# Performance work log

Hardware: AMD Instinct MI355X
Metric: run time of the kernel (lower is better)

## Reference

```python
import jax, jax.numpy as jnp
import numpy as np

N_NODES = 30000
N_EDGES = 480000
N_GRAPHS = 128
D_IN = 128
D_H = 256
N_CLASSES = 60


def gcn_conv(x, src, dst, norm, W, b, num_nodes):
    # x: [N, d_in]; W: [d_out, d_in]; b: [d_out]
    h = x @ W.T                                   # [N, d_out]
    msg = h[src] * norm[:, None]                  # [E+N, d_out] gather + scale
    out = jax.ops.segment_sum(msg, dst, num_segments=num_nodes)  # scatter-add
    return out + b


def setup_inputs() -> dict:
    key = jax.random.key(0)
    ks = jax.random.split(key, 10)
    glorot = lambda k, o, i: jax.random.normal(k, (o, i), jnp.float32) * (2.0 / (o + i)) ** 0.5
    x = jax.random.normal(ks[0], (N_NODES, D_IN), jnp.float32)
    edge_index = jax.random.randint(ks[1], (2, N_EDGES), 0, N_NODES, jnp.int64)
    batch = jnp.sort(jax.random.randint(ks[2], (N_NODES,), 0, N_GRAPHS, jnp.int64))
    return {
        "x": x,
        "edge_index": edge_index,
        "batch": batch,
        "W1": glorot(ks[3], D_H, D_IN), "b1": jnp.zeros((D_H,), jnp.float32),
        "W2": glorot(ks[4], D_H, D_H),  "b2": jnp.zeros((D_H,), jnp.float32),
        "W3": glorot(ks[5], D_H, D_H),  "b3": jnp.zeros((D_H,), jnp.float32),
        "Wfc": glorot(ks[6], N_CLASSES, D_H),
        "bfc": jnp.zeros((N_CLASSES,), jnp.float32),
    }


def reference(x, edge_index, batch, W1, b1, W2, b2, W3, b3, Wfc, bfc):
    num_nodes = x.shape[0]
    # GCNConv default: add self-loops, symmetric normalization D^-1/2 A D^-1/2
    loops = jnp.arange(num_nodes, dtype=edge_index.dtype)
    src = jnp.concatenate([edge_index[0], loops])
    dst = jnp.concatenate([edge_index[1], loops])
    deg = jax.ops.segment_sum(jnp.ones_like(dst, dtype=x.dtype), dst,
                              num_segments=num_nodes)
    dinv = jnp.where(deg > 0, jax.lax.rsqrt(deg), 0.0)
    norm = dinv[src] * dinv[dst]                  # per-edge normalization

    h = jax.nn.relu(gcn_conv(x, src, dst, norm, W1, b1, num_nodes))
    h = jax.nn.relu(gcn_conv(h, src, dst, norm, W2, b2, num_nodes))
    h = jax.nn.relu(gcn_conv(h, src, dst, norm, W3, b3, num_nodes))

    # global_mean_pool over graph ids
    sums = jax.ops.segment_sum(h, batch, num_segments=N_GRAPHS)
    cnts = jax.ops.segment_sum(jnp.ones((num_nodes,), h.dtype), batch,
                               num_segments=N_GRAPHS)
    pooled = sums / jnp.maximum(cnts, 1.0)[:, None]   # [G, 256]
    return pooled @ Wfc.T + bfc                       # [G, num_classes]
```

## Files before the change

### kernel.cpp

```cpp
#include <hip/hip_runtime.h>
#include <cstdint>
#include <cstddef>

#define NN 30000
#define NE 480000
#define NG 128
#define DIN 128
#define DH 256
#define NC 60
#define CAP 64
#define P1MAX (NN * DIN / 4)

typedef _Float16 f16x8 __attribute__((ext_vector_type(8)));
typedef _Float16 half4_t __attribute__((ext_vector_type(4)));
typedef float f32x4 __attribute__((ext_vector_type(4)));

__device__ __forceinline__ void gload_lds16(const _Float16* g, _Float16* l) {
    __builtin_amdgcn_global_load_lds(
        (const __attribute__((address_space(1))) void*)g,
        (__attribute__((address_space(3))) void*)l, 16, 0, 0);
}

__global__ __launch_bounds__(256) void k_pre(const int* __restrict__ ei, int* __restrict__ cursor,
        int* __restrict__ csr_src,
        const float* __restrict__ x, _Float16* __restrict__ xh,
        const float* __restrict__ W1, const float* __restrict__ W2, const float* __restrict__ W3,
        _Float16* __restrict__ w1h, _Float16* __restrict__ w2h, _Float16* __restrict__ w3h,
        float* __restrict__ sums) {
    int i = blockIdx.x * 256 + threadIdx.x;
    if (i < NE) {
        int s = ei[i];
        int d = ei[NE + i];
        int slot = atomicAdd(&cursor[d], 1);
        if (slot < CAP) csr_src[d * CAP + slot] = s;
    }
    if (i < P1MAX) {
        float4 v = ((const float4*)x)[i];
        half4_t o;
        o[0] = (_Float16)v.x; o[1] = (_Float16)v.y;
        o[2] = (_Float16)v.z; o[3] = (_Float16)v.w;
        ((half4_t*)xh)[i] = o;
    }
    if (i < DH * DIN) w1h[i] = (_Float16)W1[i];
    if (i < DH * DH) {
        w2h[i] = (_Float16)W2[i];
        w3h[i] = (_Float16)W3[i];
    }
    if (i < NG * DH) sums[i] = 0.f;
}

template<int K>
__global__ __launch_bounds__(256) void k_agg(const _Float16* __restrict__ hin,
        _Float16* __restrict__ tout, const int* __restrict__ cnt,
        const int* __restrict__ csr_src) {
    constexpr int L = K / 8;
    constexpr int G = 64 / L;
    int node = blockIdx.x * 4 + (threadIdx.x >> 6);
    int lane = threadIdx.x & 63;
    int sub = lane / L;
    int off = lane % L;
    const _Float16* gbase = hin + off * 8;
    float acc[8];
    #pragma unroll
    for (int u = 0; u < 8; u++) acc[u] = 0.f;
    int deg = cnt[node];
    float dvd = rsqrtf((float)(deg + 1));
    int c = deg < CAP ? deg : CAP;
    int beg = node * CAP, end = beg + c;
    int e = beg;
    for (; e + 4 * G <= end; e += 4 * G) {
        int s[4]; float w[4]; f16x8 r[4];
        #pragma unroll
        for (int j = 0; j < 4; j++) s[j] = csr_src[e + j * G + sub];
        #pragma unroll
        for (int j = 0; j < 4; j++) w[j] = rsqrtf((float)(cnt[s[j]] + 1)) * dvd;
        #pragma unroll
        for (int j = 0; j < 4; j++) r[j] = *(const f16x8*)(gbase + (size_t)s[j] * K);
        #pragma unroll
        for (int j = 0; j < 4; j++)
            #pragma unroll
            for (int u = 0; u < 8; u++) acc[u] = fmaf(w[j], (float)r[j][u], acc[u]);
    }
    for (; e < end; e += G) {
        int idx = e + sub;
        int s0 = node; float w0 = 0.f;
        if (idx < end) { s0 = csr_src[idx]; w0 = rsqrtf((float)(cnt[s0] + 1)) * dvd; }
        f16x8 r0 = *(const f16x8*)(gbase + (size_t)s0 * K);
        #pragma unroll
        for (int u = 0; u < 8; u++) acc[u] = fmaf(w0, (float)r0[u], acc[u]);
    }
    {
        float sws = (sub == 0) ? dvd * dvd : 0.f;
        f16x8 rs = *(const f16x8*)(gbase + (size_t)node * K);
        #pragma unroll
        for (int u = 0; u < 8; u++) acc[u] = fmaf(sws, (float)rs[u], acc[u]);
    }
    #pragma unroll
    for (int u = 0; u < 8; u++) {
        float v = acc[u];
        #pragma unroll
        for (int m = L; m < 64; m <<= 1) v += __shfl_xor(v, m, 64);
        acc[u] = v;
    }
    if (sub == 0) {
        f16x8 o;
        #pragma unroll
        for (int u = 0; u < 8; u++) o[u] = (_Float16)acc[u];
        *(f16x8*)(tout + (size_t)node * K + off * 8) = o;
    }
}

template<int K, bool FUSE_POOL>
__global__ __launch_bounds__(256) void k_gemm(const _Float16* __restrict__ A,
        const _Float16* __restrict__ W, const float* __restrict__ bias,
        _Float16* __restrict__ Cb, const int* __restrict__ batch,
        float* __restrict__ sums) {
    __shared__ __align__(16) _Float16 lsA[64 * 32];
    __shared__ __align__(16) _Float16 lsB[64 * 32];
    int t = threadIdx.x;
    int bm = blockIdx.x * 64;
    int bn = blockIdx.y * 64;
    int lane = t & 63, wv = t >> 6;
    int wm = (wv & 1) * 32;
    int wn = (wv >> 1) * 32;
    int lm = lane & 15, q = lane >> 4;
    int r4 = t >> 2;
    int c4 = t & 3;
    int ra = bm + r4; if (ra >= NN) ra = NN - 1;
    int rb = bn + r4;

    f32x4 acc[2][2];
    #pragma unroll
    for (int i = 0; i < 2; i++)
        #pragma unroll
        for (int j = 0; j < 2; j++) acc[i][j] = (f32x4){0.f, 0.f, 0.f, 0.f};

    for (int k0 = 0; k0 < K; k0 += 32) {
        size_t ko = (size_t)k0 + c4 * 8;
        __syncthreads();
        gload_lds16(A + (size_t)ra * K + ko, lsA + t * 8);
        gload_lds16(W + (size_t)rb * K + ko, lsB + t * 8);
        __syncthreads();
        f16x8 bf[2];
        #pragma unroll
        for (int nt = 0; nt < 2; nt++)
            bf[nt] = *(const f16x8*)&lsB[(wn + nt * 16 + lm) * 32 + q * 8];
        #pragma unroll
        for (int mt = 0; mt < 2; mt++) {
            f16x8 af = *(const f16x8*)&lsA[(wm + mt * 16 + lm) * 32 + q * 8];
            #pragma unroll
            for (int nt = 0; nt < 2; nt++)
                acc[mt][nt] = __builtin_amdgcn_mfma_f32_16x16x32_f16(af, bf[nt], acc[mt][nt], 0, 0, 0);
        }
    }
    if constexpr (!FUSE_POOL) {
        #pragma unroll
        for (int mt = 0; mt < 2; mt++) {
            #pragma unroll
            for (int nt = 0; nt < 2; nt++) {
                int col = bn + wn + nt * 16 + lm;
                float bv = bias[col];
                #pragma unroll
                for (int r = 0; r < 4; r++) {
                    int row = bm + wm + mt * 16 + q * 4 + r;
                    if (row < NN) {
                        float v = fmaxf(acc[mt][nt][r] + bv, 0.f);
                        Cb[(size_t)row * 256 + col] = (_Float16)v;
                    }
                }
            }
        }
    } else {
        int gid[8];
        #pragma unroll
        for (int mt = 0; mt < 2; mt++)
            #pragma unroll
            for (int r = 0; r < 4; r++) {
                int row = bm + wm + mt * 16 + q * 4 + r;
                gid[mt * 4 + r] = (row < NN) ? batch[row] : -1;
            }
        #pragma unroll
        for (int nt = 0; nt < 2; nt++) {
            int col = bn + wn + nt * 16 + lm;
            float bv = bias[col];
            float runsum = 0.f;
            int curg = -1;
            #pragma unroll
            for (int mt = 0; mt < 2; mt++) {
                #pragma unroll
                for (int r = 0; r < 4; r++) {
                    int g = gid[mt * 4 + r];
                    if (g >= 0) {
                        float v = fmaxf(acc[mt][nt][r] + bv, 0.f);
                        if (g != curg) {
                            if (curg >= 0) atomicAdd(&sums[curg * DH + col], runsum);
                            curg = g;
                            runsum = 0.f;
                        }
                        runsum += v;
                    }
                }
            }
            if (curg >= 0) atomicAdd(&sums[curg * DH + col], runsum);
        }
    }
}

__global__ __launch_bounds__(64) void k_fc(const float* __restrict__ sums,
        const int* __restrict__ batch, const float* __restrict__ Wfc,
        const float* __restrict__ bfc, float* __restrict__ out) {
    __shared__ float p[DH];
    int g = blockIdx.x;
    int t = threadIdx.x;
    int lo = 0, hi = NN;
    while (lo < hi) { int mid = (lo + hi) >> 1; if (batch[mid] < g) lo = mid + 1; else hi = mid; }
    int start = lo;
    hi = NN;
    while (lo < hi) { int mid = (lo + hi) >> 1; if (batch[mid] < g + 1) lo = mid + 1; else hi = mid; }
    int cnt = lo - start;
    float inv = (cnt > 0) ? 1.f / (float)cnt : 0.f;
    for (int i = t; i < DH; i += 64) p[i] = sums[g * DH + i] * inv;
    __syncthreads();
    if (t < NC) {
        float a = bfc[t];
        for (int k = 0; k < DH; k++) a = fmaf(p[k], Wfc[t * DH + k], a);
        out[g * NC + t] = a;
    }
}

extern "C" void kernel_launch(void* const* d_in, const int* in_sizes, int n_in,
                              void* d_out, int out_size, void* d_ws, size_t ws_size,
                              hipStream_t stream) {
    const float* x     = (const float*)d_in[0];
    const int*   ei    = (const int*)d_in[1];
    const int*   batch = (const int*)d_in[2];
    const float* W1 = (const float*)d_in[3];
    const float* b1 = (const float*)d_in[4];
    const float* W2 = (const float*)d_in[5];
    const float* b2 = (const float*)d_in[6];
    const float* W3 = (const float*)d_in[7];
    const float* b3 = (const float*)d_in[8];
    const float* Wfc = (const float*)d_in[9];
    const float* bfc = (const float*)d_in[10];
    float* out = (float*)d_out;

    char* wp = (char*)d_ws;
    auto alloc = [&](size_t bytes) {
        char* q = wp;
        wp += (bytes + 511) & ~(size_t)511;
        return (void*)q;
    };
    int*   cursor  = (int*)alloc((size_t)NN * 4);
    int*   csr_src = (int*)alloc((size_t)NN * CAP * 4);
    float* sums    = (float*)alloc((size_t)NG * DH * 4);
    _Float16* xh   = (_Float16*)alloc((size_t)NN * DIN * 2);
    _Float16* tb   = (_Float16*)alloc((size_t)NN * DH * 2);
    _Float16* hA   = (_Float16*)alloc((size_t)NN * DH * 2);
    _Float16* hB   = (_Float16*)alloc((size_t)NN * DH * 2);
    _Float16* w1h = (_Float16*)alloc((size_t)DH * DIN * 2);
    _Float16* w2h = (_Float16*)alloc((size_t)DH * DH * 2);
    _Float16* w3h = (_Float16*)alloc((size_t)DH * DH * 2);

    hipMemsetAsync(cursor, 0, (size_t)NN * 4, stream);

    k_pre<<<(P1MAX + 255) / 256, 256, 0, stream>>>(ei, cursor, csr_src, x, xh,
                                                   W1, W2, W3, w1h, w2h, w3h, sums);

    dim3 gg((NN + 63) / 64, 4);
    k_agg<128><<<NN / 4, 256, 0, stream>>>(xh, tb, cursor, csr_src);
    k_gemm<128, false><<<gg, 256, 0, stream>>>(tb, w1h, b1, hA, nullptr, nullptr);
    k_agg<256><<<NN / 4, 256, 0, stream>>>(hA, tb, cursor, csr_src);
    k_gemm<256, false><<<gg, 256, 0, stream>>>(tb, w2h, b2, hB, nullptr, nullptr);
    k_agg<256><<<NN / 4, 256, 0, stream>>>(hB, tb, cursor, csr_src);
    k_gemm<256, true><<<gg, 256, 0, stream>>>(tb, w3h, b3, nullptr, batch, sums);

    k_fc<<<NG, 64, 0, stream>>>(sums, batch, Wfc, bfc, out);
}
```

Before: 266.1 us.

## Split feature dimension across blocks in aggregation kernel with 8 edges per wavefront

The aggregation kernel now splits each node's feature vector into 64-wide slices, each handled by its own block. Every wavefront covers 8 features per lane and processes 8 edges in parallel with a 2-deep unroll, which gives more blocks and more edge-level parallelism per node. It also switches to nontemporal loads for CSR indices and nontemporal stores for outputs. In exchange, CSR indices and degree lookups are re-read once per slice, and the single-slice wave shape gives up the wider feature coverage per lane that K=128 had before.

```diff
diff --git a/kernel.cpp b/kernel.cpp
--- a/kernel.cpp
+++ b/kernel.cpp
@@ -53,13 +53,15 @@
 __global__ __launch_bounds__(256) void k_agg(const _Float16* __restrict__ hin,
         _Float16* __restrict__ tout, const int* __restrict__ cnt,
         const int* __restrict__ csr_src) {
-    constexpr int L = K / 8;
-    constexpr int G = 64 / L;
-    int node = blockIdx.x * 4 + (threadIdx.x >> 6);
+    constexpr int SL = K / 64;
+    int bid = blockIdx.x;
+    int slice = bid % SL;
+    int nb = bid / SL;
+    int node = nb * 4 + (threadIdx.x >> 6);
     int lane = threadIdx.x & 63;
-    int sub = lane / L;
-    int off = lane % L;
-    const _Float16* gbase = hin + off * 8;
+    int sub = lane >> 3;
+    int off = lane & 7;
+    const _Float16* gbase = hin + slice * 64 + off * 8;
     float acc[8];
     #pragma unroll
     for (int u = 0; u < 8; u++) acc[u] = 0.f;
@@ -67,27 +69,25 @@
     float dvd = rsqrtf((float)(deg + 1));
     int c = deg < CAP ? deg : CAP;
     int beg = node * CAP, end = beg + c;
-    int e = beg;
-    for (; e + 4 * G <= end; e += 4 * G) {
-        int s[4]; float w[4]; f16x8 r[4];
-        #pragma unroll
-        for (int j = 0; j < 4; j++) s[j] = csr_src[e + j * G + sub];
-        #pragma unroll
-        for (int j = 0; j < 4; j++) w[j] = rsqrtf((float)(cnt[s[j]] + 1)) * dvd;
-        #pragma unroll
-        for (int j = 0; j < 4; j++) r[j] = *(const f16x8*)(gbase + (size_t)s[j] * K);
-        #pragma unroll
-        for (int j = 0; j < 4; j++)
+    for (int e = beg; e < end; e += 16) {
+        int s[2]; float w[2]; f16x8 r[2];
+        #pragma unroll
+        for (int j = 0; j < 2; j++) {
+            int idx = e + j * 8 + sub;
+            s[j] = (idx < end) ? __builtin_nontemporal_load(&csr_src[idx]) : node;
+        }
+        #pragma unroll
+        for (int j = 0; j < 2; j++)
+            r[j] = *(const f16x8*)(gbase + (size_t)s[j] * K);
+        #pragma unroll
+        for (int j = 0; j < 2; j++) {
+            int idx = e + j * 8 + sub;
+            w[j] = (idx < end) ? rsqrtf((float)(cnt[s[j]] + 1)) * dvd : 0.f;
+        }
+        #pragma unroll
+        for (int j = 0; j < 2; j++)
             #pragma unroll
             for (int u = 0; u < 8; u++) acc[u] = fmaf(w[j], (float)r[j][u], acc[u]);
-    }
-    for (; e < end; e += G) {
-        int idx = e + sub;
-        int s0 = node; float w0 = 0.f;
-        if (idx < end) { s0 = csr_src[idx]; w0 = rsqrtf((float)(cnt[s0] + 1)) * dvd; }
-        f16x8 r0 = *(const f16x8*)(gbase + (size_t)s0 * K);
-        #pragma unroll
-        for (int u = 0; u < 8; u++) acc[u] = fmaf(w0, (float)r0[u], acc[u]);
     }
     {
         float sws = (sub == 0) ? dvd * dvd : 0.f;
@@ -99,14 +99,14 @@
     for (int u = 0; u < 8; u++) {
         float v = acc[u];
         #pragma unroll
-        for (int m = L; m < 64; m <<= 1) v += __shfl_xor(v, m, 64);
+        for (int m = 8; m < 64; m <<= 1) v += __shfl_xor(v, m, 64);
         acc[u] = v;
     }
     if (sub == 0) {
         f16x8 o;
         #pragma unroll
         for (int u = 0; u < 8; u++) o[u] = (_Float16)acc[u];
-        *(f16x8*)(tout + (size_t)node * K + off * 8) = o;
+        __builtin_nontemporal_store(o, (f16x8*)(tout + (size_t)node * K + slice * 64 + off * 8));
     }
 }
 
@@ -267,11 +267,11 @@
                                                    W1, W2, W3, w1h, w2h, w3h, sums);
 
     dim3 gg((NN + 63) / 64, 4);
-    k_agg<128><<<NN / 4, 256, 0, stream>>>(xh, tb, cursor, csr_src);
+    k_agg<128><<<(NN / 4) * 2, 256, 0, stream>>>(xh, tb, cursor, csr_src);
     k_gemm<128, false><<<gg, 256, 0, stream>>>(tb, w1h, b1, hA, nullptr, nullptr);
-    k_agg<256><<<NN / 4, 256, 0, stream>>>(hA, tb, cursor, csr_src);
+    k_agg<256><<<(NN / 4) * 4, 256, 0, stream>>>(hA, tb, cursor, csr_src);
     k_gemm<256, false><<<gg, 256, 0, stream>>>(tb, w2h, b2, hB, nullptr, nullptr);
-    k_agg<256><<<NN / 4, 256, 0, stream>>>(hB, tb, cursor, csr_src);
+    k_agg<256><<<(NN / 4) * 4, 256, 0, stream>>>(hB, tb, cursor, csr_src);
     k_gemm<256, true><<<gg, 256, 0, stream>>>(tb, w3h, b3, nullptr, batch, sums);
 
     k_fc<<<NG, 64, 0, stream>>>(sums, batch, Wfc, bfc, out);
```

After: 326.0 us. 22.5% more time.
